# Performance work log

Hardware: AMD Instinct MI355X
Metric: run time of the kernel (lower is better)

Reference implementation:

```python
import jax, jax.numpy as jnp
import numpy as np

NU, NI, E, NNZ, NLAYERS, TOPK = 2560, 3584, 64, 200000, 2, 5
N = NU + NI
DQK = 4 * E  # Linear(dim, 4*dim)


def setup_inputs() -> dict:
    key = jax.random.key(0)
    ks = jax.random.split(key, 14)
    s = 1.0 / np.sqrt(E)
    return {
        "user_emb": jax.random.normal(ks[0], (NU, E), jnp.float32) * s,
        "item_emb": jax.random.normal(ks[1], (NI, E), jnp.float32) * s,
        "norm_rows": jax.random.randint(ks[2], (NNZ,), 0, N, jnp.int32),
        "norm_cols": jax.random.randint(ks[3], (NNZ,), 0, N, jnp.int32),
        "norm_vals": jax.random.uniform(ks[4], (NNZ,), jnp.float32) / 32.0,
        "adj_rows": jax.random.randint(ks[5], (NNZ,), 0, N, jnp.int32),
        "adj_cols": jax.random.randint(ks[6], (NNZ,), 0, N, jnp.int32),
        "adj_vals": jnp.ones((NNZ,), jnp.float32),
        "Wq": jax.random.normal(ks[7], (DQK, E), jnp.float32) * s,
        "bq": jnp.zeros((DQK,), jnp.float32),
        "Wk": jax.random.normal(ks[8], (DQK, E), jnp.float32) * s,
        "bk": jnp.zeros((DQK,), jnp.float32),
        "Wv": jax.random.normal(ks[9], (DQK, E), jnp.float32) * s,
        "bv": jnp.zeros((DQK,), jnp.float32),
    }


def reference(user_emb, item_emb, norm_rows, norm_cols, norm_vals,
              adj_rows, adj_cols, adj_vals, Wq, bq, Wk, bk, Wv, bv):
    # densified sparse adjacencies (duplicates accumulated, as COO spmm would)
    A_norm = jnp.zeros((N, N), jnp.float32).at[norm_rows, norm_cols].add(norm_vals)
    A = jnp.zeros((N, N), jnp.float32).at[adj_rows, adj_cols].add(adj_vals)

    ego = jnp.concatenate([user_emb, item_emb], axis=0)  # [N, E]
    layers = []
    att_out = None
    for _ in range(NLAYERS):
        layers.append(ego)
        # GNN propagation: sparse.mm(norm_adj, ego)
        ego = A_norm @ ego  # [N, E]
        # dense similarity + sparse-blended similarity
        sim = ego @ ego.T                      # [N, N]
        sim = sim + 0.5 * (A @ sim)            # [N, N]
        # top-K neighbor selection + gather
        _, idx = jax.lax.top_k(sim, TOPK)      # [N, K]
        sample = ego[idx]                      # [N, K, E]
        # SampleAttention: Linear(dim, 4*dim) Q/K/V, scaled dot-product over K neighbors
        q = ego @ Wq.T + bq                    # [N, 4E]
        kk = sample @ Wk.T + bk                # [N, K, 4E]
        vv = sample @ Wv.T + bv                # [N, K, 4E]
        scores = jnp.einsum('nd,nkd->nk', q, kk) / jnp.sqrt(jnp.float32(DQK))
        att = jax.nn.softmax(scores, axis=-1)
        att_out = jnp.einsum('nk,nkd->nd', att, vv)  # [N, 4E]
    mean_emb = jnp.mean(jnp.stack(layers, axis=1), axis=1)  # [N, E]
    return mean_emb[:NU], mean_emb[NU:], att_out
```

## Files before the change

### kernel.cpp

```cpp
#include <hip/hip_runtime.h>
#include <math.h>

#define NUSER 2560
#define NITEM 3584
#define NN    6144
#define EDIM  64
#define NNZ   200000
#define DQK   256
#define KTOP  5
#define SPLITS 16
#define TPS    3
#define CK     8
#define ELLW   96
#define TPB   256
#define NBUILD 1563
#define BSTR  72

typedef __attribute__((ext_vector_type(8))) short bf16x8;
typedef __attribute__((ext_vector_type(4))) float f32x4;

__device__ __forceinline__ unsigned short f2bf(float f) {
    unsigned int b = __float_as_uint(f);
    unsigned int r = (b + 0x7FFFu + ((b >> 16) & 1u)) >> 16;
    return (unsigned short)r;
}
__device__ __forceinline__ int pack2(float a, float b) {
    return (int)f2bf(a) | ((int)f2bf(b) << 16);
}
__device__ __forceinline__ void ell_unpack(long long v, int* col, float* w) {
    *col = (int)(v & 0xffffffffLL);
    *w   = __int_as_float((int)(v >> 32));
}

__global__ void build_kernel(const int* __restrict__ nr, const int* __restrict__ nc,
                             const float* __restrict__ nv,
                             const int* __restrict__ ar, const int* __restrict__ ac,
                             const float* __restrict__ Wq, const float* __restrict__ Wk,
                             const float* __restrict__ bq,
                             int* __restrict__ cnt_n, int* __restrict__ cnt_a,
                             long long* __restrict__ cv_n, int* __restrict__ cv_a,
                             float* __restrict__ Gbuf) {
    int t = threadIdx.x;

    if (blockIdx.x >= NBUILD) {
        int gb = blockIdx.x - NBUILD;
        if (gb < 16) {
            int ei = gb * 4 + (t >> 6);
            int f  = t & 63;
            float a8[8];
#pragma unroll
            for (int u = 0; u < 8; ++u) a8[u] = 0.f;
            for (int d0 = 0; d0 < DQK; d0 += 8) {
#pragma unroll
                for (int u = 0; u < 8; ++u)
                    a8[u] = fmaf(Wq[(d0 + u) * 64 + ei], Wk[(d0 + u) * 64 + f], a8[u]);
            }
            Gbuf[ei * 64 + f] = ((a8[0] + a8[1]) + (a8[2] + a8[3]))
                              + ((a8[4] + a8[5]) + (a8[6] + a8[7]));
        } else {
            __shared__ float sm[256];
            int f = t & 63, dq = t >> 6;
            float p = 0.f;
            for (int d = dq * 64; d < dq * 64 + 64; ++d)
                p = fmaf(bq[d], Wk[d * 64 + f], p);
            sm[t] = p;
            __syncthreads();
            if (t < 64) Gbuf[4096 + t] = ((sm[t] + sm[64 + t]) + (sm[128 + t] + sm[192 + t]));
        }
        return;
    }

    int g = blockIdx.x * TPB + t;
    if (g < NNZ) {
        int r = nr[g], c = nc[g];
        float v = nv[g];
        int slot = atomicAdd(&cnt_n[r], 1);
        long long pk = (unsigned int)c | ((long long)(unsigned int)__float_as_int(v) << 32);
        cv_n[r * ELLW + slot] = pk;
    } else if (g < 2 * NNZ) {
        int h = g - NNZ;
        int r = ar[h], c = ac[h];
        int slot = atomicAdd(&cnt_a[r], 1);
        cv_a[r * ELLW + slot] = c;
    }
}

__global__ __launch_bounds__(TPB) void spmm_ell_emb_kernel(
        const int* __restrict__ cnt, const long long* __restrict__ cv,
        const float* __restrict__ user, const float* __restrict__ item,
        float* __restrict__ dst) {
    int r = blockIdx.x * 4 + (threadIdx.x >> 6);
    int lane = threadIdx.x & 63;
    int s = r * ELLW, e = s + cnt[r];
    float a[8];
#pragma unroll
    for (int u = 0; u < 8; ++u) a[u] = 0.f;
    int j = s, n8 = s + ((e - s) & ~7);
    for (; j < n8; j += 8) {
        int col[8]; float w[8];
#pragma unroll
        for (int u = 0; u < 8; ++u) ell_unpack(cv[j + u], &col[u], &w[u]);
#pragma unroll
        for (int u = 0; u < 8; ++u) {
            float x = (col[u] < NUSER) ? user[col[u] * EDIM + lane]
                                       : item[(col[u] - NUSER) * EDIM + lane];
            a[u] = fmaf(w[u], x, a[u]);
        }
    }
    for (; j < e; ++j) {
        int col; float w;
        ell_unpack(cv[j], &col, &w);
        float x = (col < NUSER) ? user[col * EDIM + lane] : item[(col - NUSER) * EDIM + lane];
        a[0] = fmaf(w, x, a[0]);
    }
    dst[r * EDIM + lane] = ((a[0] + a[1]) + (a[2] + a[3])) + ((a[4] + a[5]) + (a[6] + a[7]));
}

__global__ __launch_bounds__(TPB) void spmm_ell_kernel(
        const int* __restrict__ cnt, const long long* __restrict__ cv,
        const float* __restrict__ src, float* __restrict__ dst) {
    int r = blockIdx.x * 4 + (threadIdx.x >> 6);
    int lane = threadIdx.x & 63;
    int s = r * ELLW, e = s + cnt[r];
    float a[8];
#pragma unroll
    for (int u = 0; u < 8; ++u) a[u] = 0.f;
    int j = s, n8 = s + ((e - s) & ~7);
    for (; j < n8; j += 8) {
        int col[8]; float w[8];
#pragma unroll
        for (int u = 0; u < 8; ++u) ell_unpack(cv[j + u], &col[u], &w[u]);
#pragma unroll
        for (int u = 0; u < 8; ++u)
            a[u] = fmaf(w[u], src[col[u] * EDIM + lane], a[u]);
    }
    for (; j < e; ++j) {
        int col; float w;
        ell_unpack(cv[j], &col, &w);
        a[0] = fmaf(w, src[col * EDIM + lane], a[0]);
    }
    dst[r * EDIM + lane] = ((a[0] + a[1]) + (a[2] + a[3])) + ((a[4] + a[5]) + (a[6] + a[7]));
}

__global__ __launch_bounds__(TPB) void qm_mean_kernel(
        const int* __restrict__ cnt, const int* __restrict__ cv,
        const float* __restrict__ ego2, const float* __restrict__ ego1,
        const float* __restrict__ user, const float* __restrict__ item,
        const float* __restrict__ Gbuf,
        float* __restrict__ Qm, float* __restrict__ outmean, float* __restrict__ P) {
    __shared__ float Gs[4160];
    int t = threadIdx.x;

    if (blockIdx.x >= NN / 4) {
        int pb = blockIdx.x - NN / 4;
#pragma unroll
        for (int i = 0; i < 17; ++i) {
            int v = i * 256 + t;
            if (v < 4160) Gs[v] = Gbuf[v];
        }
        __syncthreads();
        int r = pb * 64 + (t >> 2), fb = (t & 3) * 16;
        const float4* row4 = (const float4*)(ego2 + (size_t)r * EDIM);
        float4 rw[16];
#pragma unroll
        for (int i = 0; i < 16; ++i) rw[i] = row4[i];
        float4 acc0 = *(const float4*)&Gs[4096 + fb];
        float4 acc1 = *(const float4*)&Gs[4096 + fb + 4];
        float4 acc2 = *(const float4*)&Gs[4096 + fb + 8];
        float4 acc3 = *(const float4*)&Gs[4096 + fb + 12];
#pragma unroll
        for (int ee = 0; ee < 16; ++ee) {
            float av[4] = {rw[ee].x, rw[ee].y, rw[ee].z, rw[ee].w};
#pragma unroll
            for (int q = 0; q < 4; ++q) {
                int e = ee * 4 + q;
                float a = av[q];
                float4 g0 = *(const float4*)&Gs[e * 64 + fb];
                float4 g1 = *(const float4*)&Gs[e * 64 + fb + 4];
                float4 g2 = *(const float4*)&Gs[e * 64 + fb + 8];
                float4 g3 = *(const float4*)&Gs[e * 64 + fb + 12];
                acc0.x = fmaf(a, g0.x, acc0.x); acc0.y = fmaf(a, g0.y, acc0.y);
                acc0.z = fmaf(a, g0.z, acc0.z); acc0.w = fmaf(a, g0.w, acc0.w);
                acc1.x = fmaf(a, g1.x, acc1.x); acc1.y = fmaf(a, g1.y, acc1.y);
                acc1.z = fmaf(a, g1.z, acc1.z); acc1.w = fmaf(a, g1.w, acc1.w);
                acc2.x = fmaf(a, g2.x, acc2.x); acc2.y = fmaf(a, g2.y, acc2.y);
                acc2.z = fmaf(a, g2.z, acc2.z); acc2.w = fmaf(a, g2.w, acc2.w);
                acc3.x = fmaf(a, g3.x, acc3.x); acc3.y = fmaf(a, g3.y, acc3.y);
                acc3.z = fmaf(a, g3.z, acc3.z); acc3.w = fmaf(a, g3.w, acc3.w);
            }
        }
        float4* dst = (float4*)(P + (size_t)r * EDIM + fb);
        dst[0] = acc0; dst[1] = acc1; dst[2] = acc2; dst[3] = acc3;
        return;
    }

    int r = blockIdx.x * 4 + (t >> 6);
    int lane = t & 63;
    int s = r * ELLW, e = s + cnt[r];
    float a[8];
#pragma unroll
    for (int u = 0; u < 8; ++u) a[u] = 0.f;
    int j = s, n8 = s + ((e - s) & ~7);
    for (; j < n8; j += 8) {
        int col[8];
#pragma unroll
        for (int u = 0; u < 8; ++u) col[u] = cv[j + u];
#pragma unroll
        for (int u = 0; u < 8; ++u)
            a[u] += ego2[col[u] * EDIM + lane];
    }
    for (; j < e; ++j) a[0] += ego2[cv[j] * EDIM + lane];
    float acc = ((a[0] + a[1]) + (a[2] + a[3])) + ((a[4] + a[5]) + (a[6] + a[7]));
    int o = r * EDIM + lane;
    Qm[o] = ego2[o] + 0.5f * acc;
    float e0v = (r < NUSER) ? user[o] : item[o - NUSER * EDIM];
    outmean[o] = 0.5f * (e0v + ego1[o]);
}

__device__ __forceinline__ void ins3(float v, int ci, float tv[3], int ti[3]) {
    if (v > tv[2]) {
        bool p1 = v > tv[1], p0 = v > tv[0];
        tv[2] = p1 ? tv[1] : v;  ti[2] = p1 ? ti[1] : ci;
        if (p1) { tv[1] = p0 ? tv[0] : v; ti[1] = p0 ? ti[0] : ci; }
        if (p0) { tv[0] = v; ti[0] = ci; }
    }
}

__global__ __launch_bounds__(TPB, 6) void topk_kernel(
        const float* __restrict__ ego2, const float* __restrict__ Qm,
        int* __restrict__ pidx) {
    __shared__ __align__(16) short smem[13312];
    int t = threadIdx.x;
    int rb = blockIdx.x % 96, sp = blockIdx.x / 96;
    int r0 = rb * 64;
    int w = t >> 6, lane = t & 63, lq = lane >> 4, lc = lane & 15;

    short* Ah = smem;
    short* Bh = smem + 4096;

    {
        int row = t >> 2, seg = t & 3;
        const float4* src = (const float4*)&Qm[(size_t)(r0 + row) * EDIM + seg * 16];
        float4 f0 = src[0], f1 = src[1], f2 = src[2], f3 = src[3];
        int4 p0, p1;
        p0.x = pack2(f0.x, f0.y); p0.y = pack2(f0.z, f0.w);
        p0.z = pack2(f1.x, f1.y); p0.w = pack2(f1.z, f1.w);
        p1.x = pack2(f2.x, f2.y); p1.y = pack2(f2.z, f2.w);
        p1.z = pack2(f3.x, f3.y); p1.w = pack2(f3.z, f3.w);
        *(int4*)&Ah[row * EDIM + seg * 16] = p0;
        *(int4*)&Ah[row * EDIM + seg * 16 + 8] = p1;
    }

    float4 pa[4], pb[4];
    {
        int c0 = (sp * TPS) * 128;
#pragma unroll
        for (int rep = 0; rep < 4; ++rep) {
            int v = t + 256 * rep;
            const float4* src = (const float4*)&ego2[(size_t)(c0 + (v >> 3)) * EDIM + (v & 7) * 8];
            pa[rep] = src[0]; pb[rep] = src[1];
        }
    }

    float t3v[4][3]; int t3i[4][3];
#pragma unroll
    for (int i = 0; i < 4; ++i)
#pragma unroll
        for (int k = 0; k < 3; ++k) { t3v[i][k] = -INFINITY; t3i[i][k] = 0x7fffffff; }

    bf16x8 af0, af1;
    for (int tile = 0; tile < TPS; ++tile) {
        int c0 = (sp * TPS + tile) * 128;
        __syncthreads();
        {
#pragma unroll
            for (int rep = 0; rep < 4; ++rep) {
                int v = t + 256 * rep;
                int4 q;
                q.x = pack2(pa[rep].x, pa[rep].y); q.y = pack2(pa[rep].z, pa[rep].w);
                q.z = pack2(pb[rep].x, pb[rep].y); q.w = pack2(pb[rep].z, pb[rep].w);
                *(int4*)&Bh[(v >> 3) * BSTR + (v & 7) * 8] = q;
            }
        }
        if (tile + 1 < TPS) {
            int c1 = c0 + 128;
#pragma unroll
            for (int rep = 0; rep < 4; ++rep) {
                int v = t + 256 * rep;
                const float4* src = (const float4*)&ego2[(size_t)(c1 + (v >> 3)) * EDIM + (v & 7) * 8];
                pa[rep] = src[0]; pb[rep] = src[1];
            }
        }
        __syncthreads();
        if (tile == 0) {
            af0 = *(const bf16x8*)&Ah[(w * 16 + lc) * EDIM + lq * 8];
            af1 = *(const bf16x8*)&Ah[(w * 16 + lc) * EDIM + 32 + lq * 8];
        }

#pragma unroll
        for (int ch = 0; ch < 8; ++ch) {
            bf16x8 b0 = *(const bf16x8*)&Bh[(ch * 16 + lc) * BSTR + lq * 8];
            bf16x8 b1 = *(const bf16x8*)&Bh[(ch * 16 + lc) * BSTR + 32 + lq * 8];
            f32x4 acc = {0.f, 0.f, 0.f, 0.f};
            acc = __builtin_amdgcn_mfma_f32_16x16x32_bf16(af0, b0, acc, 0, 0, 0);
            acc = __builtin_amdgcn_mfma_f32_16x16x32_bf16(af1, b1, acc, 0, 0, 0);
            int ci = c0 + ch * 16 + lc;
#pragma unroll
            for (int reg = 0; reg < 4; ++reg)
                ins3(acc[reg], ci, t3v[reg], t3i[reg]);
        }
    }

#pragma unroll
    for (int i = 0; i < 4; ++i) {
        int row = r0 + w * 16 + lq * 4 + i;
        int ptr = 0;
        for (int k = 0; k < CK; ++k) {
            float cvv = (ptr == 0) ? t3v[i][0] : (ptr == 1) ? t3v[i][1]
                      : (ptr == 2) ? t3v[i][2] : -INFINITY;
            int   cii = (ptr == 0) ? t3i[i][0] : (ptr == 1) ? t3i[i][1]
                      : (ptr == 2) ? t3i[i][2] : 0x7fffffff;
            float bv = cvv; int bi = cii;
#pragma unroll
            for (int off = 1; off < 16; off <<= 1) {
                float ov = __shfl_xor(bv, off, 64);
                int   oi = __shfl_xor(bi, off, 64);
                if (ov > bv || (ov == bv && oi < bi)) { bv = ov; bi = oi; }
            }
            if (bv == cvv && bi == cii) ptr++;
            if (lc == 0) pidx[(row * SPLITS + sp) * CK + k] = bi;
        }
    }
}

__global__ __launch_bounds__(TPB) void attn_sel_kernel(
        const float* __restrict__ Qm, const float* __restrict__ P,
        const float* __restrict__ ego2, const int* __restrict__ pidx,
        const float* __restrict__ Wv, const float* __restrict__ bv_,
        float* __restrict__ out) {
    __shared__ float sb[4][128];
    __shared__ float sa[4][128];
    __shared__ float smm[4][64];
    __shared__ float WvT[64 * 130];
    int wv = threadIdx.x >> 6, lane = threadIdx.x & 63;
    int t = threadIdx.x;
    int r = blockIdx.x * 4 + wv;
    int ci0 = pidx[r * 128 + lane];
    int ci1 = pidx[r * 128 + 64 + lane];
    int part = lane & 3;

    const float4* qmp = (const float4*)(Qm + (size_t)r * EDIM + part * 16);
    float4 q0 = qmp[0], q1 = qmp[1], q2 = qmp[2], q3 = qmp[3];
    const float4* pmp = (const float4*)(P + (size_t)r * EDIM + part * 16);
    float4 p0 = pmp[0], p1 = pmp[1], p2 = pmp[2], p3 = pmp[3];

#pragma unroll
    for (int p = 0; p < 8; ++p) {
        int j = p * 16 + (lane >> 2);
        int c = (j < 64) ? __shfl(ci0, j, 64) : __shfl(ci1, j - 64, 64);
        const float4* ep = (const float4*)(ego2 + (size_t)c * EDIM + part * 16);
        float4 e0 = ep[0], e1 = ep[1], e2 = ep[2], e3 = ep[3];
        float s = 0.f, s2 = 0.f;
        s = fmaf(q0.x, e0.x, s); s = fmaf(q0.y, e0.y, s); s = fmaf(q0.z, e0.z, s); s = fmaf(q0.w, e0.w, s);
        s = fmaf(q1.x, e1.x, s); s = fmaf(q1.y, e1.y, s); s = fmaf(q1.z, e1.z, s); s = fmaf(q1.w, e1.w, s);
        s = fmaf(q2.x, e2.x, s); s = fmaf(q2.y, e2.y, s); s = fmaf(q2.z, e2.z, s); s = fmaf(q2.w, e2.w, s);
        s = fmaf(q3.x, e3.x, s); s = fmaf(q3.y, e3.y, s); s = fmaf(q3.z, e3.z, s); s = fmaf(q3.w, e3.w, s);
        s2 = fmaf(p0.x, e0.x, s2); s2 = fmaf(p0.y, e0.y, s2); s2 = fmaf(p0.z, e0.z, s2); s2 = fmaf(p0.w, e0.w, s2);
        s2 = fmaf(p1.x, e1.x, s2); s2 = fmaf(p1.y, e1.y, s2); s2 = fmaf(p1.z, e1.z, s2); s2 = fmaf(p1.w, e1.w, s2);
        s2 = fmaf(p2.x, e2.x, s2); s2 = fmaf(p2.y, e2.y, s2); s2 = fmaf(p2.z, e2.z, s2); s2 = fmaf(p2.w, e2.w, s2);
        s2 = fmaf(p3.x, e3.x, s2); s2 = fmaf(p3.y, e3.y, s2); s2 = fmaf(p3.z, e3.z, s2); s2 = fmaf(p3.w, e3.w, s2);
        s  += __shfl_xor(s, 1, 64);  s  += __shfl_xor(s, 2, 64);
        s2 += __shfl_xor(s2, 1, 64); s2 += __shfl_xor(s2, 2, 64);
        if (part == 0) { sb[wv][j] = s; sa[wv][j] = s2; }
    }
    float sv0 = sb[wv][lane],      av0 = sa[wv][lane];
    float sv1 = sb[wv][64 + lane], av1 = sa[wv][64 + lane];

    float prevv = INFINITY; int previ = -1;
    int cI[KTOP]; float atk[KTOP];
#pragma unroll
    for (int k = 0; k < KTOP; ++k) {
        bool adm0 = (sv0 < prevv) || (sv0 == prevv && ci0 > previ);
        bool adm1 = (sv1 < prevv) || (sv1 == prevv && ci1 > previ);
        float bv = adm0 ? sv0 : -INFINITY;
        int   bi = adm0 ? ci0 : 0x7fffffff;
        float ba = av0;
        if (adm1 && (sv1 > bv || (sv1 == bv && ci1 < bi))) { bv = sv1; bi = ci1; ba = av1; }
#pragma unroll
        for (int off = 1; off < 64; off <<= 1) {
            float ov = __shfl_xor(bv, off, 64);
            int   oi = __shfl_xor(bi, off, 64);
            float oa = __shfl_xor(ba, off, 64);
            if (ov > bv || (ov == bv && oi < bi)) { bv = ov; bi = oi; ba = oa; }
        }
        cI[k] = bi; atk[k] = ba; prevv = bv; previ = bi;
    }

    float sc[KTOP];
#pragma unroll
    for (int k = 0; k < KTOP; ++k) sc[k] = atk[k] * 0.0625f;
    float mx = sc[0];
#pragma unroll
    for (int k = 1; k < KTOP; ++k) mx = fmaxf(mx, sc[k]);
    float wgt[KTOP], ssum = 0.f;
#pragma unroll
    for (int k = 0; k < KTOP; ++k) { wgt[k] = expf(sc[k] - mx); ssum += wgt[k]; }
    float inv = 1.f / ssum;

    float mm = 0.f;
#pragma unroll
    for (int k = 0; k < KTOP; ++k)
        mm = fmaf(wgt[k] * inv, ego2[(size_t)cI[k] * EDIM + lane], mm);
    smm[wv][lane] = mm;

    int dl = lane * 2;
#pragma unroll
    for (int pass = 0; pass < 2; ++pass) {
        __syncthreads();
#pragma unroll
        for (int i = 0; i < 8; ++i) {
            int idx = i * 256 + t;
            int d  = idx >> 4;
            int e4 = (idx & 15) * 4;
            float4 wv4 = *(const float4*)&Wv[(size_t)(pass * 128 + d) * EDIM + e4];
            WvT[(e4 + 0) * 130 + d] = wv4.x;
            WvT[(e4 + 1) * 130 + d] = wv4.y;
            WvT[(e4 + 2) * 130 + d] = wv4.z;
            WvT[(e4 + 3) * 130 + d] = wv4.w;
        }
        __syncthreads();
        float2 acc = *(const float2*)&bv_[pass * 128 + dl];
#pragma unroll 8
        for (int e = 0; e < 64; ++e) {
            float me = smm[wv][e];
            float2 wv2 = *(const float2*)&WvT[e * 130 + dl];
            acc.x = fmaf(me, wv2.x, acc.x);
            acc.y = fmaf(me, wv2.y, acc.y);
        }
        *(float2*)&out[(size_t)r * DQK + pass * 128 + dl] = acc;
    }
}

extern "C" void kernel_launch(void* const* d_in, const int* in_sizes, int n_in,
                              void* d_out, int out_size, void* d_ws, size_t ws_size,
                              hipStream_t stream) {
    const float* user  = (const float*)d_in[0];
    const float* item  = (const float*)d_in[1];
    const int*   nrows = (const int*)d_in[2];
    const int*   ncols = (const int*)d_in[3];
    const float* nvals = (const float*)d_in[4];
    const int*   arows = (const int*)d_in[5];
    const int*   acols = (const int*)d_in[6];
    const float* Wq = (const float*)d_in[8];  const float* bq = (const float*)d_in[9];
    const float* Wk = (const float*)d_in[10];
    const float* Wv = (const float*)d_in[12]; const float* bvp = (const float*)d_in[13];
    float* out = (float*)d_out;
    float* ws  = (float*)d_ws;

    const int NE = NN * EDIM;
    float* ego1 = ws;
    float* ego2 = ws + NE;
    float* Qm   = ws + 2 * NE;
    float* P    = ws + 3 * NE;
    int*   pidx = (int*)(ws + 4 * NE);
    float* Gbuf = ws + 6 * NE;
    int*   ell  = (int*)(ws + 6 * NE + 4160);
    int* cnt_n  = ell;
    int* cnt_a  = ell + 6144;
    long long* cv_n = (long long*)(ell + 12288);
    int* cv_a   = (int*)(cv_n + NN * ELLW);

    hipMemsetAsync(cnt_n, 0, 12288 * sizeof(int), stream);
    build_kernel<<<NBUILD + 17, TPB, 0, stream>>>(nrows, ncols, nvals, arows, acols,
                                                  Wq, Wk, bq,
                                                  cnt_n, cnt_a, cv_n, cv_a, Gbuf);
    spmm_ell_emb_kernel<<<NN / 4, TPB, 0, stream>>>(cnt_n, cv_n, user, item, ego1);
    spmm_ell_kernel<<<NN / 4, TPB, 0, stream>>>(cnt_n, cv_n, ego1, ego2);
    qm_mean_kernel<<<NN / 4 + 96, TPB, 0, stream>>>(cnt_a, cv_a, ego2, ego1, user, item,
                                                    Gbuf, Qm, out, P);
    topk_kernel<<<96 * SPLITS, TPB, 0, stream>>>(ego2, Qm, pidx);
    attn_sel_kernel<<<NN / 4, TPB, 0, stream>>>(Qm, P, ego2, pidx, Wv, bvp, out + NE);
}
```

Measured before the change: 224.6 us.

## Fuse P projection into attention kernel and simplify top-k merge state

Removes the extra P-computing blocks from qm_mean_kernel and instead computes each row's projection inside attn_sel_kernel. Each block stages the G matrix in shared memory, and each wave does a shuffle-based matvec, so the P buffer is no longer written to and read back from global memory. The top-k merge loop now keeps the candidate list as shifting registers instead of a pointer with selects, and bf16 packing uses the HIP intrinsic. In exchange, every attention block reloads the 4160-float G matrix and reuses the shared staging buffer for Wv.

Result: no change. 221.7 us (-1.3%).

```diff
diff --git a/kernel.cpp b/kernel.cpp
--- a/kernel.cpp
+++ b/kernel.cpp
@@ -1,4 +1,5 @@
 #include <hip/hip_runtime.h>
+#include <hip/hip_bf16.h>
 #include <math.h>
 
 #define NUSER 2560
@@ -19,13 +20,9 @@
 typedef __attribute__((ext_vector_type(8))) short bf16x8;
 typedef __attribute__((ext_vector_type(4))) float f32x4;
 
-__device__ __forceinline__ unsigned short f2bf(float f) {
-    unsigned int b = __float_as_uint(f);
-    unsigned int r = (b + 0x7FFFu + ((b >> 16) & 1u)) >> 16;
-    return (unsigned short)r;
-}
 __device__ __forceinline__ int pack2(float a, float b) {
-    return (int)f2bf(a) | ((int)f2bf(b) << 16);
+    __hip_bfloat162 h = __float22bfloat162_rn(float2{a, b});
+    return *(int*)&h;
 }
 __device__ __forceinline__ void ell_unpack(long long v, int* col, float* w) {
     *col = (int)(v & 0xffffffffLL);
@@ -146,54 +143,8 @@
         const int* __restrict__ cnt, const int* __restrict__ cv,
         const float* __restrict__ ego2, const float* __restrict__ ego1,
         const float* __restrict__ user, const float* __restrict__ item,
-        const float* __restrict__ Gbuf,
-        float* __restrict__ Qm, float* __restrict__ outmean, float* __restrict__ P) {
-    __shared__ float Gs[4160];
+        float* __restrict__ Qm, float* __restrict__ outmean) {
     int t = threadIdx.x;
-
-    if (blockIdx.x >= NN / 4) {
-        int pb = blockIdx.x - NN / 4;
-#pragma unroll
-        for (int i = 0; i < 17; ++i) {
-            int v = i * 256 + t;
-            if (v < 4160) Gs[v] = Gbuf[v];
-        }
-        __syncthreads();
-        int r = pb * 64 + (t >> 2), fb = (t & 3) * 16;
-        const float4* row4 = (const float4*)(ego2 + (size_t)r * EDIM);
-        float4 rw[16];
-#pragma unroll
-        for (int i = 0; i < 16; ++i) rw[i] = row4[i];
-        float4 acc0 = *(const float4*)&Gs[4096 + fb];
-        float4 acc1 = *(const float4*)&Gs[4096 + fb + 4];
-        float4 acc2 = *(const float4*)&Gs[4096 + fb + 8];
-        float4 acc3 = *(const float4*)&Gs[4096 + fb + 12];
-#pragma unroll
-        for (int ee = 0; ee < 16; ++ee) {
-            float av[4] = {rw[ee].x, rw[ee].y, rw[ee].z, rw[ee].w};
-#pragma unroll
-            for (int q = 0; q < 4; ++q) {
-                int e = ee * 4 + q;
-                float a = av[q];
-                float4 g0 = *(const float4*)&Gs[e * 64 + fb];
-                float4 g1 = *(const float4*)&Gs[e * 64 + fb + 4];
-                float4 g2 = *(const float4*)&Gs[e * 64 + fb + 8];
-                float4 g3 = *(const float4*)&Gs[e * 64 + fb + 12];
-                acc0.x = fmaf(a, g0.x, acc0.x); acc0.y = fmaf(a, g0.y, acc0.y);
-                acc0.z = fmaf(a, g0.z, acc0.z); acc0.w = fmaf(a, g0.w, acc0.w);
-                acc1.x = fmaf(a, g1.x, acc1.x); acc1.y = fmaf(a, g1.y, acc1.y);
-                acc1.z = fmaf(a, g1.z, acc1.z); acc1.w = fmaf(a, g1.w, acc1.w);
-                acc2.x = fmaf(a, g2.x, acc2.x); acc2.y = fmaf(a, g2.y, acc2.y);
-                acc2.z = fmaf(a, g2.z, acc2.z); acc2.w = fmaf(a, g2.w, acc2.w);
-                acc3.x = fmaf(a, g3.x, acc3.x); acc3.y = fmaf(a, g3.y, acc3.y);
-                acc3.z = fmaf(a, g3.z, acc3.z); acc3.w = fmaf(a, g3.w, acc3.w);
-            }
-        }
-        float4* dst = (float4*)(P + (size_t)r * EDIM + fb);
-        dst[0] = acc0; dst[1] = acc1; dst[2] = acc2; dst[3] = acc3;
-        return;
-    }
-
     int r = blockIdx.x * 4 + (t >> 6);
     int lane = t & 63;
     int s = r * ELLW, e = s + cnt[r];
@@ -314,34 +265,33 @@
 #pragma unroll
     for (int i = 0; i < 4; ++i) {
         int row = r0 + w * 16 + lq * 4 + i;
-        int ptr = 0;
+        float h0 = t3v[i][0], h1 = t3v[i][1], h2 = t3v[i][2];
+        int   j0 = t3i[i][0], j1 = t3i[i][1], j2 = t3i[i][2];
         for (int k = 0; k < CK; ++k) {
-            float cvv = (ptr == 0) ? t3v[i][0] : (ptr == 1) ? t3v[i][1]
-                      : (ptr == 2) ? t3v[i][2] : -INFINITY;
-            int   cii = (ptr == 0) ? t3i[i][0] : (ptr == 1) ? t3i[i][1]
-                      : (ptr == 2) ? t3i[i][2] : 0x7fffffff;
-            float bv = cvv; int bi = cii;
+            float bv = h0; int bi = j0;
 #pragma unroll
             for (int off = 1; off < 16; off <<= 1) {
                 float ov = __shfl_xor(bv, off, 64);
                 int   oi = __shfl_xor(bi, off, 64);
                 if (ov > bv || (ov == bv && oi < bi)) { bv = ov; bi = oi; }
             }
-            if (bv == cvv && bi == cii) ptr++;
+            bool cons = (bv == h0 && bi == j0);
+            if (cons) { h0 = h1; j0 = j1; h1 = h2; j1 = j2; h2 = -INFINITY; j2 = 0x7fffffff; }
             if (lc == 0) pidx[(row * SPLITS + sp) * CK + k] = bi;
         }
     }
 }
 
 __global__ __launch_bounds__(TPB) void attn_sel_kernel(
-        const float* __restrict__ Qm, const float* __restrict__ P,
-        const float* __restrict__ ego2, const int* __restrict__ pidx,
+        const float* __restrict__ Qm, const float* __restrict__ ego2,
+        const int* __restrict__ pidx, const float* __restrict__ Gbuf,
         const float* __restrict__ Wv, const float* __restrict__ bv_,
         float* __restrict__ out) {
     __shared__ float sb[4][128];
     __shared__ float sa[4][128];
     __shared__ float smm[4][64];
-    __shared__ float WvT[64 * 130];
+    __shared__ float sqp[4][64];
+    __shared__ float stage[64 * 130];
     int wv = threadIdx.x >> 6, lane = threadIdx.x & 63;
     int t = threadIdx.x;
     int r = blockIdx.x * 4 + wv;
@@ -349,9 +299,27 @@
     int ci1 = pidx[r * 128 + 64 + lane];
     int part = lane & 3;
 
+    {
+#pragma unroll
+        for (int i = 0; i < 17; ++i) {
+            int v = i * 256 + t;
+            if (v < 4160) stage[v] = Gbuf[v];
+        }
+    }
+    __syncthreads();
+
+    {
+        float qv = ego2[(size_t)r * EDIM + lane];
+        float pr = stage[4096 + lane];
+#pragma unroll 8
+        for (int e = 0; e < 64; ++e)
+            pr = fmaf(__shfl(qv, e, 64), stage[e * 64 + lane], pr);
+        sqp[wv][lane] = pr;
+    }
+
     const float4* qmp = (const float4*)(Qm + (size_t)r * EDIM + part * 16);
     float4 q0 = qmp[0], q1 = qmp[1], q2 = qmp[2], q3 = qmp[3];
-    const float4* pmp = (const float4*)(P + (size_t)r * EDIM + part * 16);
+    const float4* pmp = (const float4*)&sqp[wv][part * 16];
     float4 p0 = pmp[0], p1 = pmp[1], p2 = pmp[2], p3 = pmp[3];
 
 #pragma unroll
@@ -423,17 +391,17 @@
             int d  = idx >> 4;
             int e4 = (idx & 15) * 4;
             float4 wv4 = *(const float4*)&Wv[(size_t)(pass * 128 + d) * EDIM + e4];
-            WvT[(e4 + 0) * 130 + d] = wv4.x;
-            WvT[(e4 + 1) * 130 + d] = wv4.y;
-            WvT[(e4 + 2) * 130 + d] = wv4.z;
-            WvT[(e4 + 3) * 130 + d] = wv4.w;
+            stage[(e4 + 0) * 130 + d] = wv4.x;
+            stage[(e4 + 1) * 130 + d] = wv4.y;
+            stage[(e4 + 2) * 130 + d] = wv4.z;
+            stage[(e4 + 3) * 130 + d] = wv4.w;
         }
         __syncthreads();
         float2 acc = *(const float2*)&bv_[pass * 128 + dl];
 #pragma unroll 8
         for (int e = 0; e < 64; ++e) {
             float me = smm[wv][e];
-            float2 wv2 = *(const float2*)&WvT[e * 130 + dl];
+            float2 wv2 = *(const float2*)&stage[e * 130 + dl];
             acc.x = fmaf(me, wv2.x, acc.x);
             acc.y = fmaf(me, wv2.y, acc.y);
         }
@@ -461,10 +429,9 @@
     float* ego1 = ws;
     float* ego2 = ws + NE;
     float* Qm   = ws + 2 * NE;
-    float* P    = ws + 3 * NE;
-    int*   pidx = (int*)(ws + 4 * NE);
-    float* Gbuf = ws + 6 * NE;
-    int*   ell  = (int*)(ws + 6 * NE + 4160);
+    int*   pidx = (int*)(ws + 3 * NE);
+    float* Gbuf = ws + 5 * NE;
+    int*   ell  = (int*)(ws + 5 * NE + 4160);
     int* cnt_n  = ell;
     int* cnt_a  = ell + 6144;
     long long* cv_n = (long long*)(ell + 12288);
@@ -476,8 +443,7 @@
                                                   cnt_n, cnt_a, cv_n, cv_a, Gbuf);
     spmm_ell_emb_kernel<<<NN / 4, TPB, 0, stream>>>(cnt_n, cv_n, user, item, ego1);
     spmm_ell_kernel<<<NN / 4, TPB, 0, stream>>>(cnt_n, cv_n, ego1, ego2);
-    qm_mean_kernel<<<NN / 4 + 96, TPB, 0, stream>>>(cnt_a, cv_a, ego2, ego1, user, item,
-                                                    Gbuf, Qm, out, P);
+    qm_mean_kernel<<<NN / 4, TPB, 0, stream>>>(cnt_a, cv_a, ego2, ego1, user, item, Qm, out);
     topk_kernel<<<96 * SPLITS, TPB, 0, stream>>>(ego2, Qm, pidx);
-    attn_sel_kernel<<<NN / 4, TPB, 0, stream>>>(Qm, P, ego2, pidx, Wv, bvp, out + NE);
-}
+    attn_sel_kernel<<<NN / 4, TPB, 0, stream>>>(Qm, ego2, pidx, Gbuf, Wv, bvp, out + NE);
+}
```
